# Kernel tuning notes

Measured on AMD Instinct MI355X. Metric: run time of the kernel, lower is better.

## Reference

```python
import jax, jax.numpy as jnp
import numpy as np

N, E, B = 50000, 800000, 512
DIN, H, G, M = 128, 128, 32, 128
EPS = 1e-5


def _gcn_layer(h, src, dst, W, b):
    h = h @ W  # [N, H]
    loop = jnp.arange(N)
    s = jnp.concatenate([src, loop])
    d = jnp.concatenate([dst, loop])
    deg = jax.ops.segment_sum(jnp.ones(s.shape, h.dtype), d, num_segments=N)
    dinv = jax.lax.rsqrt(jnp.maximum(deg, 1.0))  # deg >= 1 due to self-loops
    norm = dinv[s] * dinv[d]  # [E+N]
    out = jax.ops.segment_sum(norm[:, None] * h[s], d, num_segments=N)
    return out + b


def _bn_relu(h, gamma, beta):
    mu = jnp.mean(h, axis=0)
    var = jnp.mean((h - mu) ** 2, axis=0)
    return jax.nn.relu((h - mu) * jax.lax.rsqrt(var + EPS) * gamma + beta)


def setup_inputs() -> dict:
    key = jax.random.key(0)
    ks = jax.random.split(key, 20)
    inp = {
        "x": jax.random.normal(ks[0], (N, DIN), jnp.float32),
        "edge_index": jax.random.randint(ks[1], (2, E), 0, N),
        "batch": jnp.sort(jax.random.randint(ks[2], (N,), 0, B)),
        "global_feats": jax.random.normal(ks[3], (B, G), jnp.float32),
    }
    dims = [DIN, H, H]
    for i in range(3):
        inp[f"W{i}"] = jax.random.normal(ks[4 + i], (dims[i], H), jnp.float32) / np.sqrt(dims[i])
        inp[f"b{i}"] = jnp.zeros((H,), jnp.float32)
        inp[f"g{i}"] = jnp.ones((H,), jnp.float32)
        inp[f"be{i}"] = jnp.zeros((H,), jnp.float32)
    inp["M1w"] = jax.random.normal(ks[10], (H + G, M), jnp.float32) / np.sqrt(H + G)
    inp["M1b"] = jnp.zeros((M,), jnp.float32)
    inp["M2w"] = jax.random.normal(ks[11], (M, M // 2), jnp.float32) / np.sqrt(M)
    inp["M2b"] = jnp.zeros((M // 2,), jnp.float32)
    inp["M3w"] = jax.random.normal(ks[12], (M // 2, 1), jnp.float32) / np.sqrt(M // 2)
    inp["M3b"] = jnp.zeros((1,), jnp.float32)
    return inp


def reference(x, edge_index, batch, global_feats,
              W0, b0, g0, be0, W1, b1, g1, be1, W2, b2, g2, be2,
              M1w, M1b, M2w, M2b, M3w, M3b):
    src, dst = edge_index[0], edge_index[1]
    h = x
    for W, b, g, be in ((W0, b0, g0, be0), (W1, b1, g1, be1), (W2, b2, g2, be2)):
        h = _bn_relu(_gcn_layer(h, src, dst, W, b), g, be)
    # global mean pool over graphs
    sums = jax.ops.segment_sum(h, batch, num_segments=B)  # [B, H]
    cnt = jax.ops.segment_sum(jnp.ones((N,), h.dtype), batch, num_segments=B)
    pooled = sums / jnp.maximum(cnt, 1.0)[:, None]
    z = jnp.concatenate([pooled, global_feats], axis=1)  # [B, H+G]
    z = jax.nn.relu(z @ M1w + M1b)
    z = jax.nn.relu(z @ M2w + M2b)
    out = z @ M3w + M3b  # [B, 1]
    return out.reshape(-1)
```

## Files before the change

kernel.cpp:

```cpp
#include <hip/hip_runtime.h>

#define NN 50000
#define NE 800000
#define BG 512
#define HD 128
#define GD 32
#define MD 128
#define EPSV 1e-5f
#define NBK 256
#define BSTR 196
#define BCAP 4096
#define SP 136
#define NSC 64

typedef __attribute__((ext_vector_type(8))) short bf16x8;
typedef __attribute__((ext_vector_type(4))) float f32x4;

static __device__ __forceinline__ unsigned short f2bf(float f) {
    unsigned int u = __float_as_uint(f);
    u += 0x7fffu + ((u >> 16) & 1u);
    return (unsigned short)(u >> 16);
}
static __device__ __forceinline__ float bfu(unsigned short v) {
    return __uint_as_float((unsigned int)v << 16);
}
static __device__ __forceinline__ float bf_lo(unsigned int v) {
    return __uint_as_float(v << 16);
}
static __device__ __forceinline__ float bf_hi(unsigned int v) {
    return __uint_as_float(v & 0xffff0000u);
}

__global__ __launch_bounds__(256) void k_bin(const int* __restrict__ src,
                                             const int* __restrict__ dst,
                                             int* __restrict__ bucket_cnt,
                                             unsigned int* __restrict__ binned) {
    __shared__ int hcnt[NBK];
    __shared__ int hbase[NBK];
    int tid = threadIdx.x;
    int e0 = blockIdx.x * 2048;
    unsigned int pv[8];
    int bk[8], rk[8];
#pragma unroll
    for (int i = 0; i < 8; ++i) {
        int e = e0 + i * 256 + tid;
        if (e < NE) {
            int s = src[e];
            int d = dst[e];
            bk[i] = d / BSTR;
            pv[i] = ((unsigned int)(d - bk[i] * BSTR) << 16) | (unsigned int)s;
        } else {
            bk[i] = -1;
        }
    }
    hcnt[tid] = 0;
    __syncthreads();
#pragma unroll
    for (int i = 0; i < 8; ++i)
        if (bk[i] >= 0) rk[i] = atomicAdd(&hcnt[bk[i]], 1);
    __syncthreads();
    hbase[tid] = atomicAdd(&bucket_cnt[tid], hcnt[tid]);
    __syncthreads();
#pragma unroll
    for (int i = 0; i < 8; ++i)
        if (bk[i] >= 0)
            binned[(size_t)bk[i] * BCAP + hbase[bk[i]] + rk[i]] = pv[i];
}

__global__ __launch_bounds__(256) void k_csr(const unsigned int* __restrict__ binned,
                                             const int* __restrict__ bucket_cnt,
                                             int* __restrict__ offsets,
                                             float* __restrict__ dinv,
                                             int* __restrict__ csr,
                                             const float* __restrict__ W0,
                                             const float* __restrict__ W1,
                                             const float* __restrict__ W2,
                                             unsigned short* __restrict__ Wt) {
    __shared__ unsigned short sW[128 * 130];
    __shared__ int ls[256];
    __shared__ int h[BSTR];
    __shared__ int cur[BSTR];
    __shared__ int bpre_s;
    int b = blockIdx.x, t = threadIdx.x;
    if (b >= NBK) {
        const float* Wsrc = (b == NBK) ? W0 : ((b == NBK + 1) ? W1 : W2);
#pragma unroll
        for (int i = 0; i < 64; ++i) {
            int idx = i * 256 + t;
            int k = idx >> 7, n = idx & 127;
            sW[n * 130 + k] = f2bf(Wsrc[idx]);
        }
        __syncthreads();
        unsigned short* o = Wt + (size_t)(b - NBK) * 16384;
#pragma unroll
        for (int i = 0; i < 64; ++i) {
            int idx = i * 256 + t;
            int n = idx >> 7, k = idx & 127;
            o[idx] = sW[n * 130 + k];
        }
        return;
    }
    int bc = bucket_cnt[t];
    ls[t] = bc;
    __syncthreads();
    for (int off = 1; off < 256; off <<= 1) {
        int c0 = ls[t];
        int add = (t >= off) ? ls[t - off] : 0;
        __syncthreads();
        ls[t] = c0 + add;
        __syncthreads();
    }
    if (t == b) bpre_s = ls[t] - bc;
    if (t < BSTR) h[t] = 0;
    __syncthreads();
    int bpre = bpre_s;
    int nb = bucket_cnt[b];
    const unsigned int* base = binned + (size_t)b * BCAP;
    for (int e = t; e < nb; e += 256)
        atomicAdd(&h[base[e] >> 16], 1);
    __syncthreads();
    int c = (t < BSTR) ? h[t] : 0;
    ls[t] = c;
    __syncthreads();
    for (int off = 1; off < 256; off <<= 1) {
        int c0 = ls[t];
        int add = (t >= off) ? ls[t - off] : 0;
        __syncthreads();
        ls[t] = c0 + add;
        __syncthreads();
    }
    int node = b * BSTR + t;
    if (t < BSTR) {
        int excl = ls[t] - c + bpre;
        cur[t] = excl;
        if (node < NN) {
            offsets[node] = excl;
            dinv[node] = rsqrtf((float)(c + 1));
            if (node == NN - 1) offsets[NN] = NE;
        }
    }
    __syncthreads();
    for (int e = t; e < nb; e += 256) {
        unsigned int v = base[e];
        int pos = atomicAdd(&cur[v >> 16], 1);
        csr[pos] = (int)(v & 0xffffu);
    }
}

__global__ __launch_bounds__(256) void k_gemm(const float* __restrict__ Inf,
                                              const unsigned short* __restrict__ Inh,
                                              const unsigned short* __restrict__ Wt,
                                              unsigned short* __restrict__ Th,
                                              const float* __restrict__ statsP,
                                              const float* __restrict__ gamma,
                                              const float* __restrict__ beta,
                                              const float* __restrict__ dinv,
                                              int useBN) {
    __shared__ unsigned short Abf[64 * SP];
    __shared__ unsigned short WtL[128 * SP];
    __shared__ float ssS[256];
    int tid = threadIdx.x;
    int rowBase = blockIdx.x * 64;
    if (useBN) {
        float s = 0.f;
        for (int c = 0; c < NSC; ++c) s += statsP[c * 256 + tid];
        ssS[tid] = s;
        __syncthreads();
        if (tid < 128) {
            float mu = ssS[tid] * (1.f / NN);
            float var = ssS[128 + tid] * (1.f / NN) - mu * mu;
            float sc = gamma[tid] * rsqrtf(var + EPSV);
            float sh = beta[tid] - mu * sc;
            ssS[tid] = sc;
            ssS[128 + tid] = sh;
        }
        __syncthreads();
#pragma unroll
        for (int i = 0; i < 4; ++i) {
            int q = tid + i * 256;
            int row = q >> 4;
            int k8 = (q & 15) * 8;
            int rg = rowBase + row;
            if (rg >= NN) rg = NN - 1;
            bf16x8 raw = *(const bf16x8*)&Inh[(size_t)rg * HD + k8];
            unsigned short o[8];
#pragma unroll
            for (int e = 0; e < 8; ++e) {
                float v = bfu((unsigned short)raw[e]);
                v = fmaxf(v * ssS[k8 + e] + ssS[128 + k8 + e], 0.f);
                o[e] = f2bf(v);
            }
            *(bf16x8*)&Abf[row * SP + k8] = *(bf16x8*)o;
        }
    } else {
#pragma unroll
        for (int i = 0; i < 8; ++i) {
            int q = tid + i * 256;
            int row = q >> 5;
            int c4 = (q & 31) * 4;
            int rg = rowBase + row;
            if (rg >= NN) rg = NN - 1;
            float4 v = *(const float4*)&Inf[(size_t)rg * HD + c4];
            unsigned short* p = &Abf[row * SP + c4];
            p[0] = f2bf(v.x); p[1] = f2bf(v.y); p[2] = f2bf(v.z); p[3] = f2bf(v.w);
        }
    }
#pragma unroll
    for (int i = 0; i < 8; ++i) {
        int q = tid + i * 256;
        int n = q >> 4;
        int k8 = (q & 15) * 8;
        bf16x8 w = *(const bf16x8*)&Wt[n * HD + k8];
        *(bf16x8*)&WtL[n * SP + k8] = w;
    }
    __syncthreads();
    int lane = tid & 63;
    int wv = tid >> 6;
    int quad = lane >> 4;
    int lrow = wv * 16 + (lane & 15);
    f32x4 acc[8];
#pragma unroll
    for (int c = 0; c < 8; ++c) acc[c] = (f32x4){0.f, 0.f, 0.f, 0.f};
#pragma unroll
    for (int qk = 0; qk < 4; ++qk) {
        int ko = quad * 8 + qk * 32;
        bf16x8 bfr = *(const bf16x8*)&Abf[lrow * SP + ko];
#pragma unroll
        for (int c = 0; c < 8; ++c) {
            bf16x8 afr = *(const bf16x8*)&WtL[(c * 16 + (lane & 15)) * SP + ko];
            acc[c] = __builtin_amdgcn_mfma_f32_16x16x32_bf16(afr, bfr, acc[c], 0, 0, 0);
        }
    }
    int grow = rowBase + lrow;
    if (grow < NN) {
        float di = dinv[grow];
#pragma unroll
        for (int c = 0; c < 8; ++c) {
            ushort4 o;
            o.x = f2bf(acc[c][0] * di);
            o.y = f2bf(acc[c][1] * di);
            o.z = f2bf(acc[c][2] * di);
            o.w = f2bf(acc[c][3] * di);
            *(ushort4*)&Th[(size_t)grow * HD + c * 16 + quad * 4] = o;
        }
    }
}

__global__ __launch_bounds__(256, 8) void k_aggregate(const uint4* __restrict__ T4,
                                                      const int* __restrict__ offsets,
                                                      const int* __restrict__ csr,
                                                      const float* __restrict__ dinv,
                                                      const float* __restrict__ bias,
                                                      unsigned short* __restrict__ Ah,
                                                      float* __restrict__ statsP) {
    __shared__ float sst[4][256];
    int tid = threadIdx.x;
    int wv = tid >> 6;
    int l = tid & 63;
    int half = l >> 4;
    int li = l & 15;
    *(float4*)&sst[wv][4 * l] = (float4){0.f, 0.f, 0.f, 0.f};
    int d = blockIdx.x * 4 + wv;
    if (d < NN) {
        int start = offsets[d], end = offsets[d + 1];
        float a0 = 0.f, a1 = 0.f, a2 = 0.f, a3 = 0.f;
        float a4 = 0.f, a5 = 0.f, a6 = 0.f, a7 = 0.f;
        int j = start;
        for (; j + 7 < end; j += 8) {
            int s0 = csr[j + half];
            int s1 = csr[j + 4 + half];
            uint4 v0 = T4[(size_t)s0 * 16 + li];
            uint4 v1 = T4[(size_t)s1 * 16 + li];
            a0 += bf_lo(v0.x); a1 += bf_hi(v0.x); a2 += bf_lo(v0.y); a3 += bf_hi(v0.y);
            a4 += bf_lo(v0.z); a5 += bf_hi(v0.z); a6 += bf_lo(v0.w); a7 += bf_hi(v0.w);
            a0 += bf_lo(v1.x); a1 += bf_hi(v1.x); a2 += bf_lo(v1.y); a3 += bf_hi(v1.y);
            a4 += bf_lo(v1.z); a5 += bf_hi(v1.z); a6 += bf_lo(v1.w); a7 += bf_hi(v1.w);
        }
        for (; j + 3 < end; j += 4) {
            int s0 = csr[j + half];
            uint4 v0 = T4[(size_t)s0 * 16 + li];
            a0 += bf_lo(v0.x); a1 += bf_hi(v0.x); a2 += bf_lo(v0.y); a3 += bf_hi(v0.y);
            a4 += bf_lo(v0.z); a5 += bf_hi(v0.z); a6 += bf_lo(v0.w); a7 += bf_hi(v0.w);
        }
        if (j + half < end) {
            int s0 = csr[j + half];
            uint4 v0 = T4[(size_t)s0 * 16 + li];
            a0 += bf_lo(v0.x); a1 += bf_hi(v0.x); a2 += bf_lo(v0.y); a3 += bf_hi(v0.y);
            a4 += bf_lo(v0.z); a5 += bf_hi(v0.z); a6 += bf_lo(v0.w); a7 += bf_hi(v0.w);
        }
        a0 += __shfl_xor(a0, 16); a1 += __shfl_xor(a1, 16);
        a2 += __shfl_xor(a2, 16); a3 += __shfl_xor(a3, 16);
        a4 += __shfl_xor(a4, 16); a5 += __shfl_xor(a5, 16);
        a6 += __shfl_xor(a6, 16); a7 += __shfl_xor(a7, 16);
        a0 += __shfl_xor(a0, 32); a1 += __shfl_xor(a1, 32);
        a2 += __shfl_xor(a2, 32); a3 += __shfl_xor(a3, 32);
        a4 += __shfl_xor(a4, 32); a5 += __shfl_xor(a5, 32);
        a6 += __shfl_xor(a6, 32); a7 += __shfl_xor(a7, 32);
        if (half == 0) {
            float di = dinv[d];
            uint4 vd = T4[(size_t)d * 16 + li];
            float4 bs0 = *(const float4*)&bias[8 * li];
            float4 bs1 = *(const float4*)&bias[8 * li + 4];
            float v0 = di * (a0 + bf_lo(vd.x)) + bs0.x;
            float v1 = di * (a1 + bf_hi(vd.x)) + bs0.y;
            float v2 = di * (a2 + bf_lo(vd.y)) + bs0.z;
            float v3 = di * (a3 + bf_hi(vd.y)) + bs0.w;
            float v4 = di * (a4 + bf_lo(vd.z)) + bs1.x;
            float v5 = di * (a5 + bf_hi(vd.z)) + bs1.y;
            float v6 = di * (a6 + bf_lo(vd.w)) + bs1.z;
            float v7 = di * (a7 + bf_hi(vd.w)) + bs1.w;
            int fb = 8 * li;
            *(float4*)&sst[wv][fb] = (float4){v0, v1, v2, v3};
            *(float4*)&sst[wv][fb + 4] = (float4){v4, v5, v6, v7};
            *(float4*)&sst[wv][128 + fb] = (float4){v0 * v0, v1 * v1, v2 * v2, v3 * v3};
            *(float4*)&sst[wv][128 + fb + 4] = (float4){v4 * v4, v5 * v5, v6 * v6, v7 * v7};
            unsigned short o[8];
            o[0] = f2bf(v0); o[1] = f2bf(v1); o[2] = f2bf(v2); o[3] = f2bf(v3);
            o[4] = f2bf(v4); o[5] = f2bf(v5); o[6] = f2bf(v6); o[7] = f2bf(v7);
            *(bf16x8*)&Ah[(size_t)d * HD + 8 * li] = *(bf16x8*)o;
        }
    }
    __syncthreads();
    float r = sst[0][tid] + sst[1][tid] + sst[2][tid] + sst[3][tid];
    atomicAdd(&statsP[(blockIdx.x & (NSC - 1)) * 256 + tid], r);
}

__global__ __launch_bounds__(128) void k_mlp(const unsigned short* __restrict__ Ah,
                                             const int* __restrict__ batch,
                                             const float* __restrict__ statsP,
                                             const float* __restrict__ gamma,
                                             const float* __restrict__ beta,
                                             const float* __restrict__ gfeat,
                                             const float* __restrict__ M1w,
                                             const float* __restrict__ M1b,
                                             const float* __restrict__ M2w,
                                             const float* __restrict__ M2b,
                                             const float* __restrict__ M3w,
                                             const float* __restrict__ M3b,
                                             float* __restrict__ out) {
    __shared__ int sb[2];
    __shared__ float ssc[128], ssh[128];
    __shared__ float zp[4][128];
    __shared__ float z[HD + GD];
    __shared__ float z1[MD];
    __shared__ float z2[MD / 2];
    int b = blockIdx.x, t = threadIdx.x;
    if (t < 2) {
        int val = b + t;
        int lo = 0, hi = NN;
        while (lo < hi) {
            int mid = (lo + hi) >> 1;
            if (batch[mid] < val) lo = mid + 1; else hi = mid;
        }
        sb[t] = lo;
    }
    float s = 0.f, q = 0.f;
    for (int c = 0; c < NSC; ++c) {
        s += statsP[c * 256 + t];
        q += statsP[c * 256 + 128 + t];
    }
    {
        float mu = s * (1.f / NN);
        float var = q * (1.f / NN) - mu * mu;
        float sc = gamma[t] * rsqrtf(var + EPSV);
        ssc[t] = sc;
        ssh[t] = beta[t] - mu * sc;
    }
    __syncthreads();
    int s0 = sb[0], s1 = sb[1];
    int grp = t >> 5, u = t & 31;
    float c0 = ssc[4 * u], c1 = ssc[4 * u + 1], c2 = ssc[4 * u + 2], c3 = ssc[4 * u + 3];
    float h0 = ssh[4 * u], h1 = ssh[4 * u + 1], h2 = ssh[4 * u + 2], h3 = ssh[4 * u + 3];
    float p0 = 0.f, p1 = 0.f, p2 = 0.f, p3 = 0.f;
    const uint2* A2 = (const uint2*)Ah;
    for (int r = s0 + grp; r < s1; r += 4) {
        uint2 v = A2[(size_t)r * 32 + u];
        p0 += fmaxf(bf_lo(v.x) * c0 + h0, 0.f);
        p1 += fmaxf(bf_hi(v.x) * c1 + h1, 0.f);
        p2 += fmaxf(bf_lo(v.y) * c2 + h2, 0.f);
        p3 += fmaxf(bf_hi(v.y) * c3 + h3, 0.f);
    }
    zp[grp][4 * u + 0] = p0;
    zp[grp][4 * u + 1] = p1;
    zp[grp][4 * u + 2] = p2;
    zp[grp][4 * u + 3] = p3;
    __syncthreads();
    float ic = 1.f / fmaxf((float)(s1 - s0), 1.f);
    z[t] = (zp[0][t] + zp[1][t] + zp[2][t] + zp[3][t]) * ic;
    if (t < GD) z[HD + t] = gfeat[b * GD + t];
    __syncthreads();
    float a = M1b[t];
    for (int k = 0; k < HD + GD; ++k) a += z[k] * M1w[k * MD + t];
    z1[t] = fmaxf(a, 0.f);
    __syncthreads();
    if (t < MD / 2) {
        float a2 = M2b[t];
        for (int k = 0; k < MD; ++k) a2 += z1[k] * M2w[k * (MD / 2) + t];
        z2[t] = fmaxf(a2, 0.f);
    }
    __syncthreads();
    if (t < 64) {
        float p = z2[t] * M3w[t];
#pragma unroll
        for (int off = 32; off; off >>= 1) p += __shfl_down(p, off);
        if (t == 0) out[b] = p + M3b[0];
    }
}

static inline size_t alg(size_t x) { return (x + 255) & ~(size_t)255; }

extern "C" void kernel_launch(void* const* d_in, const int* in_sizes, int n_in,
                              void* d_out, int out_size, void* d_ws, size_t ws_size,
                              hipStream_t stream) {
    const float* x = (const float*)d_in[0];
    const int* ei = (const int*)d_in[1];
    const int* batch = (const int*)d_in[2];
    const float* gf = (const float*)d_in[3];
    const float* W[3] = {(const float*)d_in[4], (const float*)d_in[8], (const float*)d_in[12]};
    const float* bb[3] = {(const float*)d_in[5], (const float*)d_in[9], (const float*)d_in[13]};
    const float* gg[3] = {(const float*)d_in[6], (const float*)d_in[10], (const float*)d_in[14]};
    const float* be[3] = {(const float*)d_in[7], (const float*)d_in[11], (const float*)d_in[15]};
    const float* M1w = (const float*)d_in[16];
    const float* M1b = (const float*)d_in[17];
    const float* M2w = (const float*)d_in[18];
    const float* M2b = (const float*)d_in[19];
    const float* M3w = (const float*)d_in[20];
    const float* M3b = (const float*)d_in[21];
    float* out = (float*)d_out;

    char* w = (char*)d_ws;
    int* bucket_cnt = (int*)w;    w += alg((size_t)NBK * 4);
    float* statsP = (float*)w;    w += alg((size_t)3 * NSC * 256 * 4);
    size_t zspan = (size_t)(w - (char*)d_ws);
    int* offsets = (int*)w;       w += alg((size_t)(NN + 1) * 4);
    int* csr = (int*)w;           w += alg((size_t)NE * 4);
    float* dinv = (float*)w;      w += alg((size_t)NN * 4);
    unsigned short* Wt = (unsigned short*)w;  w += alg((size_t)3 * 16384 * 2);
    unsigned int* binned = (unsigned int*)w;  w += alg((size_t)NBK * BCAP * 4);
    unsigned short* Ah = (unsigned short*)w;  w += alg((size_t)NN * HD * 2);
    unsigned short* Th = (unsigned short*)w;  w += alg((size_t)NN * HD * 2);

    const int* src = ei;
    const int* dst = ei + NE;

    hipMemsetAsync(bucket_cnt, 0, zspan, stream);
    k_bin<<<(NE + 2047) / 2048, 256, 0, stream>>>(src, dst, bucket_cnt, binned);
    k_csr<<<NBK + 3, 256, 0, stream>>>(binned, bucket_cnt, offsets, dinv, csr,
                                       W[0], W[1], W[2], Wt);

    for (int L = 0; L < 3; ++L) {
        k_gemm<<<(NN + 63) / 64, 256, 0, stream>>>(x, Ah, Wt + (size_t)L * 16384, Th,
                                                   statsP + (L ? (L - 1) * NSC * 256 : 0),
                                                   gg[L ? L - 1 : 0], be[L ? L - 1 : 0],
                                                   dinv, L > 0);
        k_aggregate<<<(NN + 3) / 4, 256, 0, stream>>>((const uint4*)Th, offsets, csr,
                                                      dinv, bb[L], Ah,
                                                      statsP + (size_t)L * NSC * 256);
    }

    k_mlp<<<BG, 128, 0, stream>>>(Ah, batch, statsP + (size_t)2 * NSC * 256,
                                  gg[2], be[2], gf, M1w, M1b, M2w, M2b, M3w, M3b, out);
}
```

Before: 317.6 us.

## Split aggregation into four feature chunks with chunk-major block ordering

The aggregate kernel now processes one 32-feature chunk (64 bytes) per block instead of the full 128-feature row. Each wave spreads 16 edges across its lanes, with 4 lanes per edge, and blocks are ordered chunk-major, so each pass gathers from a quarter-width slice of the feature matrix. The aim is to raise L2 hit rates on the random gathers and expose more memory parallelism. The cost is four times as many blocks, four reads of the CSR indices and offsets, extra shuffle reduction steps, and more atomics on the statistics buffer.

```diff
diff --git a/kernel.cpp b/kernel.cpp
--- a/kernel.cpp
+++ b/kernel.cpp
@@ -12,6 +12,7 @@
 #define BCAP 4096
 #define SP 136
 #define NSC 64
+#define DBLK 12500
 
 typedef __attribute__((ext_vector_type(8))) short bf16x8;
 typedef __attribute__((ext_vector_type(4))) float f32x4;
@@ -253,41 +254,61 @@
                                                       const float* __restrict__ bias,
                                                       unsigned short* __restrict__ Ah,
                                                       float* __restrict__ statsP) {
-    __shared__ float sst[4][256];
+    __shared__ float sst[4][64];
     int tid = threadIdx.x;
     int wv = tid >> 6;
     int l = tid & 63;
-    int half = l >> 4;
-    int li = l & 15;
-    *(float4*)&sst[wv][4 * l] = (float4){0.f, 0.f, 0.f, 0.f};
-    int d = blockIdx.x * 4 + wv;
+    int half = l >> 2;
+    int li = l & 3;
+    sst[wv][l] = 0.f;
+    int chunk = blockIdx.x / DBLK;
+    int dblock = blockIdx.x - chunk * DBLK;
+    int cbase = chunk * 4;
+    int d = dblock * 4 + wv;
     if (d < NN) {
         int start = offsets[d], end = offsets[d + 1];
+        uint4 vd = T4[(size_t)d * 16 + cbase + li];
         float a0 = 0.f, a1 = 0.f, a2 = 0.f, a3 = 0.f;
         float a4 = 0.f, a5 = 0.f, a6 = 0.f, a7 = 0.f;
         int j = start;
-        for (; j + 7 < end; j += 8) {
+        for (; j + 63 < end; j += 64) {
             int s0 = csr[j + half];
-            int s1 = csr[j + 4 + half];
-            uint4 v0 = T4[(size_t)s0 * 16 + li];
-            uint4 v1 = T4[(size_t)s1 * 16 + li];
+            int s1 = csr[j + 16 + half];
+            int s2 = csr[j + 32 + half];
+            int s3 = csr[j + 48 + half];
+            uint4 v0 = T4[(size_t)s0 * 16 + cbase + li];
+            uint4 v1 = T4[(size_t)s1 * 16 + cbase + li];
+            uint4 v2 = T4[(size_t)s2 * 16 + cbase + li];
+            uint4 v3 = T4[(size_t)s3 * 16 + cbase + li];
             a0 += bf_lo(v0.x); a1 += bf_hi(v0.x); a2 += bf_lo(v0.y); a3 += bf_hi(v0.y);
             a4 += bf_lo(v0.z); a5 += bf_hi(v0.z); a6 += bf_lo(v0.w); a7 += bf_hi(v0.w);
             a0 += bf_lo(v1.x); a1 += bf_hi(v1.x); a2 += bf_lo(v1.y); a3 += bf_hi(v1.y);
             a4 += bf_lo(v1.z); a5 += bf_hi(v1.z); a6 += bf_lo(v1.w); a7 += bf_hi(v1.w);
-        }
-        for (; j + 3 < end; j += 4) {
+            a0 += bf_lo(v2.x); a1 += bf_hi(v2.x); a2 += bf_lo(v2.y); a3 += bf_hi(v2.y);
+            a4 += bf_lo(v2.z); a5 += bf_hi(v2.z); a6 += bf_lo(v2.w); a7 += bf_hi(v2.w);
+            a0 += bf_lo(v3.x); a1 += bf_hi(v3.x); a2 += bf_lo(v3.y); a3 += bf_hi(v3.y);
+            a4 += bf_lo(v3.z); a5 += bf_hi(v3.z); a6 += bf_lo(v3.w); a7 += bf_hi(v3.w);
+        }
+        for (; j + 15 < end; j += 16) {
             int s0 = csr[j + half];
-            uint4 v0 = T4[(size_t)s0 * 16 + li];
+            uint4 v0 = T4[(size_t)s0 * 16 + cbase + li];
             a0 += bf_lo(v0.x); a1 += bf_hi(v0.x); a2 += bf_lo(v0.y); a3 += bf_hi(v0.y);
             a4 += bf_lo(v0.z); a5 += bf_hi(v0.z); a6 += bf_lo(v0.w); a7 += bf_hi(v0.w);
         }
         if (j + half < end) {
             int s0 = csr[j + half];
-            uint4 v0 = T4[(size_t)s0 * 16 + li];
+            uint4 v0 = T4[(size_t)s0 * 16 + cbase + li];
             a0 += bf_lo(v0.x); a1 += bf_hi(v0.x); a2 += bf_lo(v0.y); a3 += bf_hi(v0.y);
             a4 += bf_lo(v0.z); a5 += bf_hi(v0.z); a6 += bf_lo(v0.w); a7 += bf_hi(v0.w);
         }
+        a0 += __shfl_xor(a0, 4);  a1 += __shfl_xor(a1, 4);
+        a2 += __shfl_xor(a2, 4);  a3 += __shfl_xor(a3, 4);
+        a4 += __shfl_xor(a4, 4);  a5 += __shfl_xor(a5, 4);
+        a6 += __shfl_xor(a6, 4);  a7 += __shfl_xor(a7, 4);
+        a0 += __shfl_xor(a0, 8);  a1 += __shfl_xor(a1, 8);
+        a2 += __shfl_xor(a2, 8);  a3 += __shfl_xor(a3, 8);
+        a4 += __shfl_xor(a4, 8);  a5 += __shfl_xor(a5, 8);
+        a6 += __shfl_xor(a6, 8);  a7 += __shfl_xor(a7, 8);
         a0 += __shfl_xor(a0, 16); a1 += __shfl_xor(a1, 16);
         a2 += __shfl_xor(a2, 16); a3 += __shfl_xor(a3, 16);
         a4 += __shfl_xor(a4, 16); a5 += __shfl_xor(a5, 16);
@@ -298,9 +319,9 @@
         a6 += __shfl_xor(a6, 32); a7 += __shfl_xor(a7, 32);
         if (half == 0) {
             float di = dinv[d];
-            uint4 vd = T4[(size_t)d * 16 + li];
-            float4 bs0 = *(const float4*)&bias[8 * li];
-            float4 bs1 = *(const float4*)&bias[8 * li + 4];
+            int fb = chunk * 32 + 8 * li;
+            float4 bs0 = *(const float4*)&bias[fb];
+            float4 bs1 = *(const float4*)&bias[fb + 4];
             float v0 = di * (a0 + bf_lo(vd.x)) + bs0.x;
             float v1 = di * (a1 + bf_hi(vd.x)) + bs0.y;
             float v2 = di * (a2 + bf_lo(vd.y)) + bs0.z;
@@ -309,20 +330,24 @@
             float v5 = di * (a5 + bf_hi(vd.z)) + bs1.y;
             float v6 = di * (a6 + bf_lo(vd.w)) + bs1.z;
             float v7 = di * (a7 + bf_hi(vd.w)) + bs1.w;
-            int fb = 8 * li;
-            *(float4*)&sst[wv][fb] = (float4){v0, v1, v2, v3};
-            *(float4*)&sst[wv][fb + 4] = (float4){v4, v5, v6, v7};
-            *(float4*)&sst[wv][128 + fb] = (float4){v0 * v0, v1 * v1, v2 * v2, v3 * v3};
-            *(float4*)&sst[wv][128 + fb + 4] = (float4){v4 * v4, v5 * v5, v6 * v6, v7 * v7};
+            int sb = 8 * li;
+            *(float4*)&sst[wv][sb] = (float4){v0, v1, v2, v3};
+            *(float4*)&sst[wv][sb + 4] = (float4){v4, v5, v6, v7};
+            *(float4*)&sst[wv][32 + sb] = (float4){v0 * v0, v1 * v1, v2 * v2, v3 * v3};
+            *(float4*)&sst[wv][32 + sb + 4] = (float4){v4 * v4, v5 * v5, v6 * v6, v7 * v7};
             unsigned short o[8];
             o[0] = f2bf(v0); o[1] = f2bf(v1); o[2] = f2bf(v2); o[3] = f2bf(v3);
             o[4] = f2bf(v4); o[5] = f2bf(v5); o[6] = f2bf(v6); o[7] = f2bf(v7);
-            *(bf16x8*)&Ah[(size_t)d * HD + 8 * li] = *(bf16x8*)o;
-        }
-    }
-    __syncthreads();
-    float r = sst[0][tid] + sst[1][tid] + sst[2][tid] + sst[3][tid];
-    atomicAdd(&statsP[(blockIdx.x & (NSC - 1)) * 256 + tid], r);
+            *(bf16x8*)&Ah[(size_t)d * HD + fb] = *(bf16x8*)o;
+        }
+    }
+    __syncthreads();
+    if (tid < 64) {
+        float r = sst[0][tid] + sst[1][tid] + sst[2][tid] + sst[3][tid];
+        int part = tid >> 5;
+        int f = chunk * 32 + (tid & 31);
+        atomicAdd(&statsP[(blockIdx.x & (NSC - 1)) * 256 + part * 128 + f], r);
+    }
 }
 
 __global__ __launch_bounds__(128) void k_mlp(const unsigned short* __restrict__ Ah,
@@ -453,9 +478,9 @@
                                                    statsP + (L ? (L - 1) * NSC * 256 : 0),
                                                    gg[L ? L - 1 : 0], be[L ? L - 1 : 0],
                                                    dinv, L > 0);
-        k_aggregate<<<(NN + 3) / 4, 256, 0, stream>>>((const uint4*)Th, offsets, csr,
-                                                      dinv, bb[L], Ah,
-                                                      statsP + (size_t)L * NSC * 256);
+        k_aggregate<<<4 * DBLK, 256, 0, stream>>>((const uint4*)Th, offsets, csr,
+                                                  dinv, bb[L], Ah,
+                                                  statsP + (size_t)L * NSC * 256);
     }
 
     k_mlp<<<BG, 128, 0, stream>>>(Ah, batch, statsP + (size_t)2 * NSC * 256,
```

Result: slower. 479.6 us (+51.0%).
